# Optimization experiments

Measured on AMD Instinct MI355X. Metric: run time of the kernel, lower is better.

## Reference

```python
import jax, jax.numpy as jnp
import numpy as np

EMB = 1024
HEADS = 16
HEAD_SZ = 64
INNER = 4 * EMB
EPS = 1e-5


def layer_norm(x, g, b):
    mu = jnp.mean(x, axis=-1, keepdims=True)
    var = jnp.mean(jnp.square(x - mu), axis=-1, keepdims=True)
    return (x - mu) * jax.lax.rsqrt(var + EPS) * g + b


def setup_inputs() -> dict:
    key = jax.random.key(0)
    ks = jax.random.split(key, 12)
    s = 1.0 / np.sqrt(EMB)
    si = 1.0 / np.sqrt(INNER)
    return {
        "x": jax.random.normal(ks[0], (4, 2048, EMB), dtype=jnp.float32),
        "Wq": jax.random.uniform(ks[1], (EMB, HEADS * HEAD_SZ), jnp.float32, -s, s),
        "Wk": jax.random.uniform(ks[2], (EMB, HEADS * HEAD_SZ), jnp.float32, -s, s),
        "Wv": jax.random.uniform(ks[3], (EMB, HEADS * HEAD_SZ), jnp.float32, -s, s),
        "Wo": jax.random.uniform(ks[4], (HEADS * HEAD_SZ, EMB), jnp.float32, -s, s),
        "bo": jax.random.uniform(ks[5], (EMB,), jnp.float32, -s, s),
        "g1": jnp.ones((EMB,), jnp.float32),
        "b1": jnp.zeros((EMB,), jnp.float32),
        "W1": jax.random.uniform(ks[6], (EMB, INNER), jnp.float32, -s, s),
        "bf1": jax.random.uniform(ks[7], (INNER,), jnp.float32, -s, s),
        "W2": jax.random.uniform(ks[8], (INNER, EMB), jnp.float32, -si, si),
        "bf2": jax.random.uniform(ks[9], (EMB,), jnp.float32, -si, si),
        "g2": jnp.ones((EMB,), jnp.float32),
        "b2": jnp.zeros((EMB,), jnp.float32),
    }


def reference(x, Wq, Wk, Wv, Wo, bo, g1, b1, W1, bf1, W2, bf2, g2, b2):
    bs, seq, _ = x.shape
    # QKV projections -> [b, h, s, d]
    def split_heads(t):
        return t.reshape(bs, seq, HEADS, HEAD_SZ).transpose(0, 2, 1, 3)
    q = split_heads(x @ Wq)
    k = split_heads(x @ Wk)
    v = split_heads(x @ Wv)
    # scaled dot-product attention (vanilla, no mask; pdrop=0)
    attn = jnp.einsum("bhqd,bhkd->bhqk", q, k) / np.sqrt(HEAD_SZ)
    attn = jax.nn.softmax(attn, axis=-1)
    out = jnp.einsum("bhqk,bhkd->bhqd", attn, v)
    out = out.transpose(0, 2, 1, 3).reshape(bs, seq, HEADS * HEAD_SZ)
    out = out @ Wo + bo
    # residual + post-LN
    h = layer_norm(x + out, g1, b1)
    # FFN
    ff = jax.nn.relu(h @ W1 + bf1) @ W2 + bf2
    return layer_norm(h + ff, g2, b2)
```

## Files before the change

kernel.cpp:

```cpp
#include <hip/hip_runtime.h>
#include <stdint.h>

#define DEVI __device__ __forceinline__

typedef __attribute__((ext_vector_type(8))) short bf16x8;
typedef __attribute__((ext_vector_type(4))) float f32x4;
typedef unsigned short u16;
typedef uint32_t u32;

constexpr int EMB = 1024, SEQ = 2048, NTOK = 8192;
constexpr int HEADS = 16, HD = 64, INNER = 4096;

DEVI u16 f2b(float f) {
  u32 u = __float_as_uint(f);
  return (u16)((u + 0x7FFFu + ((u >> 16) & 1u)) >> 16);
}

DEVI u32 pk2(float lo, float hi) {
  u32 r;
  asm("v_cvt_pk_bf16_f32 %0, %1, %2" : "=v"(r) : "v"(lo), "v"(hi));
  return r;
}

DEVI float exp2v(float x) {
  float r;
  asm("v_exp_f32 %0, %1" : "=v"(r) : "v"(x));
  return r;
}

DEVI void gload16(const void* g, void* l) {
  __builtin_amdgcn_global_load_lds(
      (const __attribute__((address_space(1))) void*)g,
      (__attribute__((address_space(3))) void*)l, 16, 0, 0);
}

DEVI int xcd_swz(int bid, int nwg) { return (bid & 7) * (nwg >> 3) + (bid >> 3); }

DEVI int vperm(int k) {
  int g = (k >> 2) & 3, j = k & 3, s2 = k >> 4;
  return ((s2 >> 1) << 5) + (g << 3) + ((s2 & 1) << 2) + j;
}

__global__ __launch_bounds__(256) void k_cvt(const float* __restrict__ src,
                                             u16* __restrict__ dst, int n4) {
  int i = blockIdx.x * 256 + threadIdx.x;
  if (i >= n4) return;
  float4 v = ((const float4*)src)[i];
  ushort4 o = {f2b(v.x), f2b(v.y), f2b(v.z), f2b(v.w)};
  ((ushort4*)dst)[i] = o;
}

__global__ __launch_bounds__(256) void k_cvtT(const float* __restrict__ src,
                                              u16* __restrict__ dst, int K, int N) {
  __shared__ float t[32][33];
  int bk = blockIdx.x % (K >> 5), bn = blockIdx.x / (K >> 5);
  int tx = threadIdx.x & 31, ty = threadIdx.x >> 5;
#pragma unroll
  for (int i = 0; i < 4; i++)
    t[ty + i * 8][tx] = src[(size_t)(bk * 32 + ty + i * 8) * N + bn * 32 + tx];
  __syncthreads();
#pragma unroll
  for (int i = 0; i < 4; i++)
    dst[(size_t)(bn * 32 + ty + i * 8) * K + bk * 32 + tx] = f2b(t[tx][ty + i * 8]);
}

template <int EPI>
__global__ __launch_bounds__(512, 2) void k_g256(
    const u16* __restrict__ A, const u16* __restrict__ BT, int M, int N, int K,
    u16* __restrict__ ob0, u16* __restrict__ ob1, u16* __restrict__ ob2,
    float* __restrict__ of0, const float* __restrict__ bias,
    const float* __restrict__ res) {
  __shared__ u16 LDS[81920];
  const int tid = threadIdx.x;
  const int lane = tid & 63, w = tid >> 6;
  const int wr = w >> 2, wc = w & 3;
  const int g = lane >> 4, c = lane & 15;
  const int nbx = N >> 8;
  const int bid = xcd_swz(blockIdx.x, gridDim.x);
  const int by = bid / nbx, bx = bid % nbx;
  const int row0 = by << 8, col0 = bx << 8;
  const int NK = K >> 6;

  const f32x4 z4 = {0.f, 0.f, 0.f, 0.f};
  f32x4 acc[8][4];
#pragma unroll
  for (int m = 0; m < 8; m++)
#pragma unroll
    for (int n = 0; n < 4; n++) acc[m][n] = z4;

  auto stA = [&](int t, int h) {
    const int k0 = t << 6;
    char* base = (char*)LDS + (t % 3) * 32768 + h * 16384;
#pragma unroll
    for (int i = 0; i < 2; i++) {
      int s = tid + (i << 9);
      int r = (h << 7) + (s >> 3), cb = s & 7;
      gload16(A + (size_t)(row0 + r) * K + (k0 + ((cb ^ (r & 7)) << 3)),
              base + s * 16);
    }
  };
  auto stB = [&](int t, int h) {
    const int k0 = t << 6;
    char* base = (char*)LDS + 98304 + (t & 1) * 32768 + h * 16384;
#pragma unroll
    for (int i = 0; i < 2; i++) {
      int s = tid + (i << 9);
      int r = (h << 7) + (s >> 3), cb = s & 7;
      gload16(BT + (size_t)(col0 + r) * K + (k0 + ((cb ^ (r & 7)) << 3)),
              base + s * 16);
    }
  };
  auto rdA = [&](const char* Ab, int row, int kk) {
    return *(const bf16x8*)(Ab + ((row * 128 + kk * 64 + g * 16) ^ ((row & 7) << 4)));
  };

  stA(0, 0); stA(0, 1);
  stB(0, 0); stB(0, 1);
  stA(1, 0); stA(1, 1);
  asm volatile("s_waitcnt vmcnt(4)" ::: "memory");
  __builtin_amdgcn_s_barrier();
  __builtin_amdgcn_sched_barrier(0);

  for (int t = 0; t < NK; t++) {
    const char* Ab = (const char*)LDS + (t % 3) * 32768;
    const char* Bb = (const char*)LDS + 98304 + (t & 1) * 32768;
    bf16x8 af[4][2], b0[2][2], b1[2][2];

#pragma unroll
    for (int m = 0; m < 4; m++)
#pragma unroll
      for (int kk = 0; kk < 2; kk++) af[m][kk] = rdA(Ab, wr * 128 + m * 16 + c, kk);
#pragma unroll
    for (int n = 0; n < 2; n++)
#pragma unroll
      for (int kk = 0; kk < 2; kk++) b0[n][kk] = rdA(Bb, wc * 64 + n * 16 + c, kk);
    if (t + 1 < NK) stB(t + 1, 0);
    asm volatile("s_waitcnt lgkmcnt(8)" ::: "memory");
    __builtin_amdgcn_sched_barrier(0);
    __builtin_amdgcn_s_barrier();
    asm volatile("s_waitcnt lgkmcnt(0)" ::: "memory");
    __builtin_amdgcn_sched_barrier(0);
    __builtin_amdgcn_s_setprio(1);
#pragma unroll
    for (int m = 0; m < 4; m++)
#pragma unroll
      for (int n = 0; n < 2; n++)
#pragma unroll
        for (int kk = 0; kk < 2; kk++)
          acc[m][n] = __builtin_amdgcn_mfma_f32_16x16x32_bf16(af[m][kk], b0[n][kk],
                                                              acc[m][n], 0, 0, 0);
    __builtin_amdgcn_s_setprio(0);
    __builtin_amdgcn_sched_barrier(0);
    __builtin_amdgcn_s_barrier();

#pragma unroll
    for (int n = 0; n < 2; n++)
#pragma unroll
      for (int kk = 0; kk < 2; kk++)
        b1[n][kk] = rdA(Bb, wc * 64 + 32 + n * 16 + c, kk);
    if (t + 1 < NK) stB(t + 1, 1);
    __builtin_amdgcn_sched_barrier(0);
    __builtin_amdgcn_s_barrier();
    asm volatile("s_waitcnt lgkmcnt(0)" ::: "memory");
    __builtin_amdgcn_sched_barrier(0);
    __builtin_amdgcn_s_setprio(1);
#pragma unroll
    for (int m = 0; m < 4; m++)
#pragma unroll
      for (int n = 0; n < 2; n++)
#pragma unroll
        for (int kk = 0; kk < 2; kk++)
          acc[m][2 + n] = __builtin_amdgcn_mfma_f32_16x16x32_bf16(af[m][kk], b1[n][kk],
                                                                  acc[m][2 + n], 0, 0, 0);
    __builtin_amdgcn_s_setprio(0);
    __builtin_amdgcn_sched_barrier(0);
    __builtin_amdgcn_s_barrier();

#pragma unroll
    for (int m = 0; m < 4; m++)
#pragma unroll
      for (int kk = 0; kk < 2; kk++)
        af[m][kk] = rdA(Ab, wr * 128 + 64 + m * 16 + c, kk);
    if (t + 2 < NK) stA(t + 2, 0);
    __builtin_amdgcn_sched_barrier(0);
    __builtin_amdgcn_s_barrier();
    asm volatile("s_waitcnt lgkmcnt(0)" ::: "memory");
    __builtin_amdgcn_sched_barrier(0);
    __builtin_amdgcn_s_setprio(1);
#pragma unroll
    for (int m = 0; m < 4; m++)
#pragma unroll
      for (int n = 0; n < 2; n++)
#pragma unroll
        for (int kk = 0; kk < 2; kk++)
          acc[4 + m][n] = __builtin_amdgcn_mfma_f32_16x16x32_bf16(af[m][kk], b0[n][kk],
                                                                  acc[4 + m][n], 0, 0, 0);
    __builtin_amdgcn_s_setprio(0);
    __builtin_amdgcn_sched_barrier(0);
    __builtin_amdgcn_s_barrier();

    if (t + 2 < NK) stA(t + 2, 1);
    __builtin_amdgcn_sched_barrier(0);
    __builtin_amdgcn_s_barrier();
    __builtin_amdgcn_s_setprio(1);
#pragma unroll
    for (int m = 0; m < 4; m++)
#pragma unroll
      for (int n = 0; n < 2; n++)
#pragma unroll
        for (int kk = 0; kk < 2; kk++)
          acc[4 + m][2 + n] = __builtin_amdgcn_mfma_f32_16x16x32_bf16(
              af[m][kk], b1[n][kk], acc[4 + m][2 + n], 0, 0, 0);
    __builtin_amdgcn_s_setprio(0);
    __builtin_amdgcn_sched_barrier(0);
    if (t + 2 < NK)
      asm volatile("s_waitcnt vmcnt(4)" ::: "memory");
    else if (t + 1 < NK)
      asm volatile("s_waitcnt vmcnt(0)" ::: "memory");
    __builtin_amdgcn_s_barrier();
    __builtin_amdgcn_sched_barrier(0);
  }

#pragma unroll
  for (int m = 0; m < 8; m++) {
#pragma unroll
    for (int n = 0; n < 4; n++) {
      int ocol = col0 + wc * 64 + n * 16 + c;
      int orow_base = row0 + wr * 128 + m * 16 + 4 * g;
      if constexpr (EPI == 0) {
        int which = ocol >> 10, rem = ocol & 1023;
        int h = rem >> 6, d = rem & 63;
        if (which == 2) {
          int b = orow_base >> 11, sl = orow_base & 2047;
          int blk = sl & ~63, k4 = sl & 63;
          int p = vperm(k4);
          int bh = b * HEADS + h;
          ushort4 vv = {f2b(acc[m][n][0]), f2b(acc[m][n][1]),
                        f2b(acc[m][n][2]), f2b(acc[m][n][3])};
          *(ushort4*)(ob2 + ((size_t)bh * HD + d) * SEQ + blk + p) = vv;
        } else {
#pragma unroll
          for (int r = 0; r < 4; r++) {
            int orow = orow_base + r;
            int b = orow >> 11, s = orow & 2047;
            int bh = b * HEADS + h;
            float av = acc[m][n][r];
            if (which == 0)
              ob0[((size_t)bh * SEQ + s) * HD + d] = f2b(av * 0.1803368801111244f);
            else
              ob1[((size_t)bh * SEQ + s) * HD + d] = f2b(av);
          }
        }
      } else if constexpr (EPI == 2) {
        float bia = bias[ocol];
#pragma unroll
        for (int r = 0; r < 4; r++) {
          int orow = orow_base + r;
          float v = acc[m][n][r] + bia;
          ob0[(size_t)orow * N + ocol] = f2b(v > 0.f ? v : 0.f);
        }
      } else {
        float bia = bias[ocol];
#pragma unroll
        for (int r = 0; r < 4; r++) {
          int orow = orow_base + r;
          float v = acc[m][n][r] + bia;
          if constexpr (EPI == 1)
            of0[(size_t)orow * N + ocol] = v + res[(size_t)orow * N + ocol];
          else
            of0[(size_t)orow * N + ocol] = v;
        }
      }
    }
  }
}

template <int EPI>
__global__ __launch_bounds__(512, 2) void k_gemm8(
    const u16* __restrict__ A, const u16* __restrict__ BT, int M, int N, int K,
    u16* __restrict__ ob0, u16* __restrict__ ob1, u16* __restrict__ ob2,
    float* __restrict__ of0, const float* __restrict__ bias,
    const float* __restrict__ res) {
  __shared__ u16 LDS[3][24576];
  const int tid = threadIdx.x;
  const int lane = tid & 63, w = tid >> 6;
  const int wr = w >> 1, wc = w & 1;
  const int g = lane >> 4, c = lane & 15;
  const int nbx = N >> 7;
  const int bid = xcd_swz(blockIdx.x, gridDim.x);
  const int by = bid / nbx, bx = bid % nbx;
  const int row0 = by << 8, col0 = bx << 7;
  const int NK = K >> 6;

  const f32x4 z4 = {0.f, 0.f, 0.f, 0.f};
  f32x4 acc[4][4];
#pragma unroll
  for (int m = 0; m < 4; m++)
#pragma unroll
    for (int n = 0; n < 4; n++) acc[m][n] = z4;

  auto stageA = [&](int t) {
    const int k0 = t << 6;
    char* base = (char*)&LDS[t % 3][0];
#pragma unroll
    for (int i = 0; i < 4; i++) {
      int s = tid + (i << 9);
      int r = s >> 3, cb = s & 7;
      gload16(A + (size_t)(row0 + r) * K + (k0 + ((cb ^ (r & 7)) << 3)),
              base + s * 16);
    }
  };
  auto stageB = [&](int t) {
    const int k0 = t << 6;
    char* base = (char*)&LDS[t % 3][0] + 32768;
#pragma unroll
    for (int i = 0; i < 2; i++) {
      int s = tid + (i << 9);
      int r = s >> 3, cb = s & 7;
      gload16(BT + (size_t)(col0 + r) * K + (k0 + ((cb ^ (r & 7)) << 3)),
              base + s * 16);
    }
  };

  stageA(0); stageB(0);
  stageA(1); stageB(1);
  asm volatile("s_waitcnt vmcnt(6)" ::: "memory");
  __builtin_amdgcn_s_barrier();

  for (int t = 0; t < NK; t++) {
    const char* Ab = (const char*)&LDS[t % 3][0];
    const char* Bb = Ab + 32768;

    bf16x8 af[4][2], bfr[2][2];
#pragma unroll
    for (int m = 0; m < 4; m++)
#pragma unroll
      for (int kk = 0; kk < 2; kk++) {
        int r = wr * 64 + m * 16 + c;
        af[m][kk] = *(const bf16x8*)(Ab + ((r * 128 + kk * 64 + g * 16) ^ ((r & 7) << 4)));
      }
#pragma unroll
    for (int ni = 0; ni < 2; ni++)
#pragma unroll
      for (int kk = 0; kk < 2; kk++) {
        int rb = wc * 64 + ni * 16 + c;
        bfr[ni][kk] = *(const bf16x8*)(Bb + ((rb * 128 + kk * 64 + g * 16) ^ ((rb & 7) << 4)));
      }
    if (t + 2 < NK) stageA(t + 2);
    __builtin_amdgcn_sched_barrier(0);
    __builtin_amdgcn_s_barrier();
    asm volatile("s_waitcnt lgkmcnt(0)" ::: "memory");
    __builtin_amdgcn_sched_barrier(0);
    __builtin_amdgcn_s_setprio(1);
#pragma unroll
    for (int m = 0; m < 4; m++)
#pragma unroll
      for (int ni = 0; ni < 2; ni++)
#pragma unroll
        for (int kk = 0; kk < 2; kk++)
          acc[m][ni] = __builtin_amdgcn_mfma_f32_16x16x32_bf16(af[m][kk], bfr[ni][kk],
                                                               acc[m][ni], 0, 0, 0);
    __builtin_amdgcn_s_setprio(0);
    __builtin_amdgcn_sched_barrier(0);
    __builtin_amdgcn_s_barrier();

#pragma unroll
    for (int ni = 0; ni < 2; ni++)
#pragma unroll
      for (int kk = 0; kk < 2; kk++) {
        int rb = wc * 64 + 32 + ni * 16 + c;
        bfr[ni][kk] = *(const bf16x8*)(Bb + ((rb * 128 + kk * 64 + g * 16) ^ ((rb & 7) << 4)));
      }
    if (t + 2 < NK) stageB(t + 2);
    __builtin_amdgcn_sched_barrier(0);
    __builtin_amdgcn_s_barrier();
    asm volatile("s_waitcnt lgkmcnt(0)" ::: "memory");
    __builtin_amdgcn_sched_barrier(0);
    __builtin_amdgcn_s_setprio(1);
#pragma unroll
    for (int m = 0; m < 4; m++)
#pragma unroll
      for (int ni = 0; ni < 2; ni++)
#pragma unroll
        for (int kk = 0; kk < 2; kk++)
          acc[m][2 + ni] = __builtin_amdgcn_mfma_f32_16x16x32_bf16(af[m][kk], bfr[ni][kk],
                                                                   acc[m][2 + ni], 0, 0, 0);
    __builtin_amdgcn_s_setprio(0);
    __builtin_amdgcn_sched_barrier(0);
    if (t + 2 < NK)
      asm volatile("s_waitcnt vmcnt(6)" ::: "memory");
    else if (t + 1 < NK)
      asm volatile("s_waitcnt vmcnt(0)" ::: "memory");
    __builtin_amdgcn_s_barrier();
  }

#pragma unroll
  for (int m = 0; m < 4; m++) {
#pragma unroll
    for (int n = 0; n < 4; n++) {
      int ocol = col0 + wc * 64 + n * 16 + c;
      int orow_base = row0 + wr * 64 + m * 16 + 4 * g;
      if constexpr (EPI == 1) {
        float bia = bias[ocol];
#pragma unroll
        for (int r = 0; r < 4; r++) {
          int orow = orow_base + r;
          of0[(size_t)orow * N + ocol] =
              acc[m][n][r] + bia + res[(size_t)orow * N + ocol];
        }
      } else {
        float bia = bias[ocol];
#pragma unroll
        for (int r = 0; r < 4; r++) {
          int orow = orow_base + r;
          of0[(size_t)orow * N + ocol] = acc[m][n][r] + bia;
        }
      }
    }
  }
}

__global__ __launch_bounds__(256, 4) void k_attn(const u16* __restrict__ q,
                                                 const u16* __restrict__ kb,
                                                 const u16* __restrict__ vT,
                                                 u16* __restrict__ attn) {
  __shared__ u16 Ks[2][64 * 64];
  __shared__ u16 Vs[2][64 * 64];
  const int tid = threadIdx.x, lane = tid & 63, w = tid >> 6;
  const int g = lane >> 4, c = lane & 15;
  const int blk = xcd_swz(blockIdx.x, gridDim.x);
  const int bh = blk >> 5, qb = blk & 31;
  const int b = bh >> 4, h = bh & 15;
  const u16* qh = q + (size_t)bh * SEQ * HD;
  const u16* kh = kb + (size_t)bh * SEQ * HD;
  const u16* vh = vT + (size_t)bh * HD * SEQ;
  const int qr = qb * 64 + w * 16 + c;
  bf16x8 qf0 = *(const bf16x8*)(qh + (size_t)qr * HD + 8 * g);
  bf16x8 qf1 = *(const bf16x8*)(qh + (size_t)qr * HD + 32 + 8 * g);

  const f32x4 z4 = {0.f, 0.f, 0.f, 0.f};
  f32x4 O[4];
#pragma unroll
  for (int m = 0; m < 4; m++) O[m] = z4;
  float mI = -3.0e38f, lI = 0.f;

  auto stage = [&](int kt, int buf) {
    const int kv0 = kt * 64;
#pragma unroll
    for (int i = 0; i < 2; i++) {
      int s = tid + (i << 8);
      int r = s >> 3, cb = s & 7;
      gload16(kh + (size_t)(kv0 + r) * HD + ((cb ^ (r & 7)) << 3),
              (char*)Ks[buf] + s * 16);
    }
#pragma unroll
    for (int i = 0; i < 2; i++) {
      int s = tid + (i << 8);
      int r = s >> 3, cb = s & 7;
      gload16(vh + (size_t)r * SEQ + kv0 + ((cb ^ (r & 7)) << 3),
              (char*)Vs[buf] + s * 16);
    }
  };

  stage(0, 0);
  __syncthreads();
  int cur = 0;
  constexpr int NT = SEQ / 64;
  for (int kt = 0; kt < NT; kt++) {
    if (kt + 1 < NT) stage(kt + 1, cur ^ 1);

    const char* ksb = (const char*)Ks[cur];
    f32x4 sc[4];
    __builtin_amdgcn_s_setprio(1);
#pragma unroll
    for (int m = 0; m < 4; m++) {
      int r = 16 * m + c;
      int sw = (r & 7) << 4;
      bf16x8 kf0 = *(const bf16x8*)(ksb + ((r * 128 + g * 16) ^ sw));
      bf16x8 kf1 = *(const bf16x8*)(ksb + ((r * 128 + 64 + g * 16) ^ sw));
      f32x4 a = z4;
      a = __builtin_amdgcn_mfma_f32_16x16x32_bf16(kf0, qf0, a, 0, 0, 0);
      a = __builtin_amdgcn_mfma_f32_16x16x32_bf16(kf1, qf1, a, 0, 0, 0);
      sc[m] = a;
    }
    __builtin_amdgcn_s_setprio(0);

    float mx = sc[0][0];
#pragma unroll
    for (int m = 0; m < 4; m++)
#pragma unroll
      for (int r = 0; r < 4; r++) mx = fmaxf(mx, sc[m][r]);
    mx = fmaxf(mx, __shfl_xor(mx, 16));
    mx = fmaxf(mx, __shfl_xor(mx, 32));
    if (!__all(mx - mI <= 8.f)) {
      float mNew = fmaxf(mI, mx);
      float alpha = exp2v(mI - mNew);
      lI *= alpha;
#pragma unroll
      for (int m = 0; m < 4; m++)
#pragma unroll
        for (int r = 0; r < 4; r++) O[m][r] *= alpha;
      mI = mNew;
    }
    float p[4][4];
    float rs = 0.f;
#pragma unroll
    for (int m = 0; m < 4; m++)
#pragma unroll
      for (int r = 0; r < 4; r++) {
        p[m][r] = exp2v(sc[m][r] - mI);
        rs += p[m][r];
      }
    rs += __shfl_xor(rs, 16);
    rs += __shfl_xor(rs, 32);
    lI += rs;

    union V8w { bf16x8 v; u32 w4[4]; };
    V8w pa0, pa1;
    pa0.w4[0] = pk2(p[0][0], p[0][1]); pa0.w4[1] = pk2(p[0][2], p[0][3]);
    pa0.w4[2] = pk2(p[1][0], p[1][1]); pa0.w4[3] = pk2(p[1][2], p[1][3]);
    pa1.w4[0] = pk2(p[2][0], p[2][1]); pa1.w4[1] = pk2(p[2][2], p[2][3]);
    pa1.w4[2] = pk2(p[3][0], p[3][1]); pa1.w4[3] = pk2(p[3][2], p[3][3]);

    const char* vsb = (const char*)Vs[cur];
    __builtin_amdgcn_s_setprio(1);
#pragma unroll
    for (int m = 0; m < 4; m++) {
      int d = 16 * m + c;
      int sw = (d & 7) << 4;
      bf16x8 v0 = *(const bf16x8*)(vsb + ((d * 128 + g * 16) ^ sw));
      bf16x8 v1 = *(const bf16x8*)(vsb + ((d * 128 + 64 + g * 16) ^ sw));
      O[m] = __builtin_amdgcn_mfma_f32_16x16x32_bf16(v0, pa0.v, O[m], 0, 0, 0);
      O[m] = __builtin_amdgcn_mfma_f32_16x16x32_bf16(v1, pa1.v, O[m], 0, 0, 0);
    }
    __builtin_amdgcn_s_setprio(0);

    __syncthreads();
    cur ^= 1;
  }

  float inv = 1.f / lI;
#pragma unroll
  for (int m = 0; m < 4; m++) {
    ushort4 ov = {f2b(O[m][0] * inv), f2b(O[m][1] * inv),
                  f2b(O[m][2] * inv), f2b(O[m][3] * inv)};
    int col = h * 64 + 16 * m + 4 * g;
    *(ushort4*)(attn + ((size_t)(b * SEQ + qr)) * EMB + col) = ov;
  }
}

__global__ __launch_bounds__(256) void k_ln1(const float* __restrict__ y,
                                             const float* __restrict__ gw,
                                             const float* __restrict__ bw,
                                             float* __restrict__ hf,
                                             u16* __restrict__ hb) {
  const int row = blockIdx.x, tid = threadIdx.x, lane = tid & 63, w = tid >> 6;
  const float4 v = ((const float4*)(y + (size_t)row * EMB))[tid];
  float s = v.x + v.y + v.z + v.w;
  float s2 = v.x * v.x + v.y * v.y + v.z * v.z + v.w * v.w;
#pragma unroll
  for (int m = 1; m < 64; m <<= 1) {
    s += __shfl_xor(s, m);
    s2 += __shfl_xor(s2, m);
  }
  __shared__ float rs_[4], rq_[4];
  if (lane == 0) { rs_[w] = s; rq_[w] = s2; }
  __syncthreads();
  s = rs_[0] + rs_[1] + rs_[2] + rs_[3];
  s2 = rq_[0] + rq_[1] + rq_[2] + rq_[3];
  const float mu = s * (1.f / EMB);
  const float var = s2 * (1.f / EMB) - mu * mu;
  const float rstd = rsqrtf(var + 1e-5f);
  const float4 gg = ((const float4*)gw)[tid];
  const float4 bb = ((const float4*)bw)[tid];
  float4 o;
  o.x = (v.x - mu) * rstd * gg.x + bb.x;
  o.y = (v.y - mu) * rstd * gg.y + bb.y;
  o.z = (v.z - mu) * rstd * gg.z + bb.z;
  o.w = (v.w - mu) * rstd * gg.w + bb.w;
  ((float4*)(hf + (size_t)row * EMB))[tid] = o;
  ushort4 ob = {f2b(o.x), f2b(o.y), f2b(o.z), f2b(o.w)};
  ((ushort4*)(hb + (size_t)row * EMB))[tid] = ob;
}

__global__ __launch_bounds__(256) void k_ln2(const float* __restrict__ hf,
                                             const float* __restrict__ z,
                                             const float* __restrict__ gw,
                                             const float* __restrict__ bw,
                                             float* __restrict__ outp) {
  const int row = blockIdx.x, tid = threadIdx.x, lane = tid & 63, w = tid >> 6;
  float4 v = ((const float4*)(hf + (size_t)row * EMB))[tid];
  const float4 zz = ((const float4*)(z + (size_t)row * EMB))[tid];
  v.x += zz.x; v.y += zz.y; v.z += zz.z; v.w += zz.w;
  float s = v.x + v.y + v.z + v.w;
  float s2 = v.x * v.x + v.y * v.y + v.z * v.z + v.w * v.w;
#pragma unroll
  for (int m = 1; m < 64; m <<= 1) {
    s += __shfl_xor(s, m);
    s2 += __shfl_xor(s2, m);
  }
  __shared__ float rs_[4], rq_[4];
  if (lane == 0) { rs_[w] = s; rq_[w] = s2; }
  __syncthreads();
  s = rs_[0] + rs_[1] + rs_[2] + rs_[3];
  s2 = rq_[0] + rq_[1] + rq_[2] + rq_[3];
  const float mu = s * (1.f / EMB);
  const float var = s2 * (1.f / EMB) - mu * mu;
  const float rstd = rsqrtf(var + 1e-5f);
  const float4 gg = ((const float4*)gw)[tid];
  const float4 bb = ((const float4*)bw)[tid];
  float4 o;
  o.x = (v.x - mu) * rstd * gg.x + bb.x;
  o.y = (v.y - mu) * rstd * gg.y + bb.y;
  o.z = (v.z - mu) * rstd * gg.z + bb.z;
  o.w = (v.w - mu) * rstd * gg.w + bb.w;
  ((float4*)(outp + (size_t)row * EMB))[tid] = o;
}

extern "C" void kernel_launch(void* const* d_in, const int* in_sizes, int n_in,
                              void* d_out, int out_size, void* d_ws, size_t ws_size,
                              hipStream_t stream) {
  const float* x = (const float*)d_in[0];
  const float* Wq = (const float*)d_in[1];
  const float* Wk = (const float*)d_in[2];
  const float* Wv = (const float*)d_in[3];
  const float* Wo = (const float*)d_in[4];
  const float* bo = (const float*)d_in[5];
  const float* g1 = (const float*)d_in[6];
  const float* b1 = (const float*)d_in[7];
  const float* W1 = (const float*)d_in[8];
  const float* bf1 = (const float*)d_in[9];
  const float* W2 = (const float*)d_in[10];
  const float* bf2 = (const float*)d_in[11];
  const float* g2 = (const float*)d_in[12];
  const float* b2 = (const float*)d_in[13];
  float* out = (float*)d_out;

  char* ws = (char*)d_ws;
  size_t off = 0;
  auto alloc = [&](size_t bytes) {
    char* p = ws + off;
    off += (bytes + 255) & ~(size_t)255;
    return p;
  };
  u16* xb = (u16*)alloc((size_t)NTOK * EMB * 2);
  u16* wqkvT = (u16*)alloc((size_t)3072 * 1024 * 2);
  u16* qB = (u16*)alloc((size_t)NTOK * EMB * 2);
  u16* kB = (u16*)alloc((size_t)NTOK * EMB * 2);
  u16* vTB = (u16*)alloc((size_t)NTOK * EMB * 2);
  u16* woT = (u16*)alloc((size_t)1024 * 1024 * 2);
  u16* w1T = (u16*)alloc((size_t)4096 * 1024 * 2);
  u16* w2T = (u16*)alloc((size_t)1024 * 4096 * 2);
  float* y = (float*)alloc((size_t)NTOK * EMB * 4);
  u16* ff1 = (u16*)alloc((size_t)NTOK * INNER * 2);
  u16* attn = xb;
  float* hf = (float*)qB;
  u16* hb = vTB;
  float* z = y;

  k_cvt<<<NTOK * EMB / 4 / 256, 256, 0, stream>>>(x, xb, NTOK * EMB / 4);
  k_cvtT<<<1024, 256, 0, stream>>>(Wq, wqkvT, 1024, 1024);
  k_cvtT<<<1024, 256, 0, stream>>>(Wk, wqkvT + 1048576, 1024, 1024);
  k_cvtT<<<1024, 256, 0, stream>>>(Wv, wqkvT + 2097152, 1024, 1024);
  k_cvtT<<<1024, 256, 0, stream>>>(Wo, woT, 1024, 1024);
  k_cvtT<<<4096, 256, 0, stream>>>(W1, w1T, 1024, 4096);
  k_cvtT<<<4096, 256, 0, stream>>>(W2, w2T, 4096, 1024);
  k_g256<0><<<(NTOK / 256) * (3072 / 256), 512, 0, stream>>>(
      xb, wqkvT, NTOK, 3072, 1024, qB, kB, vTB, nullptr, nullptr, nullptr);
  k_attn<<<64 * 32, 256, 0, stream>>>(qB, kB, vTB, attn);
  k_gemm8<1><<<(NTOK / 256) * (1024 / 128), 512, 0, stream>>>(
      attn, woT, NTOK, 1024, 1024, nullptr, nullptr, nullptr, y, bo, x);
  k_ln1<<<NTOK, 256, 0, stream>>>(y, g1, b1, hf, hb);
  k_g256<2><<<(NTOK / 256) * (4096 / 256), 512, 0, stream>>>(
      hb, w1T, NTOK, 4096, 1024, ff1, nullptr, nullptr, nullptr, bf1, nullptr);
  k_gemm8<3><<<(NTOK / 256) * (1024 / 128), 512, 0, stream>>>(
      ff1, w2T, NTOK, 1024, 4096, nullptr, nullptr, nullptr, z, bf2, nullptr);
  k_ln2<<<NTOK, 256, 0, stream>>>(hf, z, g2, b2, out);
}
```

Measured before the change: 534.7 us.

## Merge prep kernels, store residual activations in bf16, and relax GEMM sched barriers

Folds the seven conversion and transpose launches into one k_prep launch. The Wo GEMM now writes x+attn as bf16 instead of fp32, and LN1 no longer writes an fp32 copy of h, so LN2 rebuilds the residual from the bf16 h. This cuts memory traffic at the cost of lower precision in the residual path. It also removes several sched_barriers and an lgkmcnt wait in the 256-tile GEMM, moves the softmax row-sum shuffles out of the attention loop, and rewrites the max reduction as a tree.

```diff
diff --git a/kernel.cpp b/kernel.cpp
--- a/kernel.cpp
+++ b/kernel.cpp
@@ -15,6 +15,7 @@
   u32 u = __float_as_uint(f);
   return (u16)((u + 0x7FFFu + ((u >> 16) & 1u)) >> 16);
 }
+DEVI float b2f(u16 h) { return __uint_as_float(((u32)h) << 16); }
 
 DEVI u32 pk2(float lo, float hi) {
   u32 r;
@@ -41,19 +42,38 @@
   return ((s2 >> 1) << 5) + (g << 3) + ((s2 & 1) << 2) + j;
 }
 
-__global__ __launch_bounds__(256) void k_cvt(const float* __restrict__ src,
-                                             u16* __restrict__ dst, int n4) {
-  int i = blockIdx.x * 256 + threadIdx.x;
-  if (i >= n4) return;
-  float4 v = ((const float4*)src)[i];
-  ushort4 o = {f2b(v.x), f2b(v.y), f2b(v.z), f2b(v.w)};
-  ((ushort4*)dst)[i] = o;
-}
-
-__global__ __launch_bounds__(256) void k_cvtT(const float* __restrict__ src,
-                                              u16* __restrict__ dst, int K, int N) {
+__global__ __launch_bounds__(256) void k_prep(
+    const float* __restrict__ x, const float* __restrict__ Wq,
+    const float* __restrict__ Wk, const float* __restrict__ Wv,
+    const float* __restrict__ Wo, const float* __restrict__ W1,
+    const float* __restrict__ W2, u16* __restrict__ xb, u16* __restrict__ wqkvT,
+    u16* __restrict__ woT, u16* __restrict__ w1T, u16* __restrict__ w2T) {
   __shared__ float t[32][33];
-  int bk = blockIdx.x % (K >> 5), bn = blockIdx.x / (K >> 5);
+  int b = blockIdx.x;
+  if (b < 8192) {
+    int i = b * 256 + threadIdx.x;
+    float4 v = ((const float4*)x)[i];
+    ushort4 o = {f2b(v.x), f2b(v.y), f2b(v.z), f2b(v.w)};
+    ((ushort4*)xb)[i] = o;
+    return;
+  }
+  b -= 8192;
+  const float* src;
+  u16* dst;
+  int K, N;
+  if (b < 4096) {
+    int m = b >> 10;
+    b &= 1023;
+    K = 1024; N = 1024;
+    src = (m == 0) ? Wq : (m == 1) ? Wk : (m == 2) ? Wv : Wo;
+    dst = (m == 0) ? wqkvT : (m == 1) ? wqkvT + 1048576
+        : (m == 2) ? wqkvT + 2097152 : woT;
+  } else if (b < 8192) {
+    b -= 4096; src = W1; dst = w1T; K = 1024; N = 4096;
+  } else {
+    b -= 8192; src = W2; dst = w2T; K = 4096; N = 1024;
+  }
+  int bk = b % (K >> 5), bn = b / (K >> 5);
   int tx = threadIdx.x & 31, ty = threadIdx.x >> 5;
 #pragma unroll
   for (int i = 0; i < 4; i++)
@@ -119,7 +139,6 @@
   stA(1, 0); stA(1, 1);
   asm volatile("s_waitcnt vmcnt(4)" ::: "memory");
   __builtin_amdgcn_s_barrier();
-  __builtin_amdgcn_sched_barrier(0);
 
   for (int t = 0; t < NK; t++) {
     const char* Ab = (const char*)LDS + (t % 3) * 32768;
@@ -135,8 +154,6 @@
 #pragma unroll
       for (int kk = 0; kk < 2; kk++) b0[n][kk] = rdA(Bb, wc * 64 + n * 16 + c, kk);
     if (t + 1 < NK) stB(t + 1, 0);
-    asm volatile("s_waitcnt lgkmcnt(8)" ::: "memory");
-    __builtin_amdgcn_sched_barrier(0);
     __builtin_amdgcn_s_barrier();
     asm volatile("s_waitcnt lgkmcnt(0)" ::: "memory");
     __builtin_amdgcn_sched_barrier(0);
@@ -150,7 +167,6 @@
           acc[m][n] = __builtin_amdgcn_mfma_f32_16x16x32_bf16(af[m][kk], b0[n][kk],
                                                               acc[m][n], 0, 0, 0);
     __builtin_amdgcn_s_setprio(0);
-    __builtin_amdgcn_sched_barrier(0);
     __builtin_amdgcn_s_barrier();
 
 #pragma unroll
@@ -159,7 +175,6 @@
       for (int kk = 0; kk < 2; kk++)
         b1[n][kk] = rdA(Bb, wc * 64 + 32 + n * 16 + c, kk);
     if (t + 1 < NK) stB(t + 1, 1);
-    __builtin_amdgcn_sched_barrier(0);
     __builtin_amdgcn_s_barrier();
     asm volatile("s_waitcnt lgkmcnt(0)" ::: "memory");
     __builtin_amdgcn_sched_barrier(0);
@@ -173,7 +188,6 @@
           acc[m][2 + n] = __builtin_amdgcn_mfma_f32_16x16x32_bf16(af[m][kk], b1[n][kk],
                                                                   acc[m][2 + n], 0, 0, 0);
     __builtin_amdgcn_s_setprio(0);
-    __builtin_amdgcn_sched_barrier(0);
     __builtin_amdgcn_s_barrier();
 
 #pragma unroll
@@ -182,7 +196,6 @@
       for (int kk = 0; kk < 2; kk++)
         af[m][kk] = rdA(Ab, wr * 128 + 64 + m * 16 + c, kk);
     if (t + 2 < NK) stA(t + 2, 0);
-    __builtin_amdgcn_sched_barrier(0);
     __builtin_amdgcn_s_barrier();
     asm volatile("s_waitcnt lgkmcnt(0)" ::: "memory");
     __builtin_amdgcn_sched_barrier(0);
@@ -196,11 +209,9 @@
           acc[4 + m][n] = __builtin_amdgcn_mfma_f32_16x16x32_bf16(af[m][kk], b0[n][kk],
                                                                   acc[4 + m][n], 0, 0, 0);
     __builtin_amdgcn_s_setprio(0);
-    __builtin_amdgcn_sched_barrier(0);
     __builtin_amdgcn_s_barrier();
 
     if (t + 2 < NK) stA(t + 2, 1);
-    __builtin_amdgcn_sched_barrier(0);
     __builtin_amdgcn_s_barrier();
     __builtin_amdgcn_s_setprio(1);
 #pragma unroll
@@ -212,13 +223,11 @@
           acc[4 + m][2 + n] = __builtin_amdgcn_mfma_f32_16x16x32_bf16(
               af[m][kk], b1[n][kk], acc[4 + m][2 + n], 0, 0, 0);
     __builtin_amdgcn_s_setprio(0);
-    __builtin_amdgcn_sched_barrier(0);
     if (t + 2 < NK)
       asm volatile("s_waitcnt vmcnt(4)" ::: "memory");
     else if (t + 1 < NK)
       asm volatile("s_waitcnt vmcnt(0)" ::: "memory");
     __builtin_amdgcn_s_barrier();
-    __builtin_amdgcn_sched_barrier(0);
   }
 
 #pragma unroll
@@ -251,7 +260,7 @@
               ob1[((size_t)bh * SEQ + s) * HD + d] = f2b(av);
           }
         }
-      } else if constexpr (EPI == 2) {
+      } else {
         float bia = bias[ocol];
 #pragma unroll
         for (int r = 0; r < 4; r++) {
@@ -259,17 +268,6 @@
           float v = acc[m][n][r] + bia;
           ob0[(size_t)orow * N + ocol] = f2b(v > 0.f ? v : 0.f);
         }
-      } else {
-        float bia = bias[ocol];
-#pragma unroll
-        for (int r = 0; r < 4; r++) {
-          int orow = orow_base + r;
-          float v = acc[m][n][r] + bia;
-          if constexpr (EPI == 1)
-            of0[(size_t)orow * N + ocol] = v + res[(size_t)orow * N + ocol];
-          else
-            of0[(size_t)orow * N + ocol] = v;
-        }
       }
     }
   }
@@ -278,8 +276,7 @@
 template <int EPI>
 __global__ __launch_bounds__(512, 2) void k_gemm8(
     const u16* __restrict__ A, const u16* __restrict__ BT, int M, int N, int K,
-    u16* __restrict__ ob0, u16* __restrict__ ob1, u16* __restrict__ ob2,
-    float* __restrict__ of0, const float* __restrict__ bias,
+    u16* __restrict__ ob0, float* __restrict__ of0, const float* __restrict__ bias,
     const float* __restrict__ res) {
   __shared__ u16 LDS[3][24576];
   const int tid = threadIdx.x;
@@ -400,21 +397,15 @@
     for (int n = 0; n < 4; n++) {
       int ocol = col0 + wc * 64 + n * 16 + c;
       int orow_base = row0 + wr * 64 + m * 16 + 4 * g;
-      if constexpr (EPI == 1) {
-        float bia = bias[ocol];
-#pragma unroll
-        for (int r = 0; r < 4; r++) {
-          int orow = orow_base + r;
-          of0[(size_t)orow * N + ocol] =
-              acc[m][n][r] + bia + res[(size_t)orow * N + ocol];
-        }
-      } else {
-        float bia = bias[ocol];
-#pragma unroll
-        for (int r = 0; r < 4; r++) {
-          int orow = orow_base + r;
+      float bia = bias[ocol];
+#pragma unroll
+      for (int r = 0; r < 4; r++) {
+        int orow = orow_base + r;
+        if constexpr (EPI == 1)
+          ob0[(size_t)orow * N + ocol] =
+              f2b(acc[m][n][r] + bia + res[(size_t)orow * N + ocol]);
+        else
           of0[(size_t)orow * N + ocol] = acc[m][n][r] + bia;
-        }
       }
     }
   }
@@ -485,11 +476,14 @@
     }
     __builtin_amdgcn_s_setprio(0);
 
-    float mx = sc[0][0];
-#pragma unroll
-    for (int m = 0; m < 4; m++)
-#pragma unroll
-      for (int r = 0; r < 4; r++) mx = fmaxf(mx, sc[m][r]);
+    float a0 = fmaxf(fmaxf(sc[0][0], sc[0][1]), sc[0][2]);
+    float a1 = fmaxf(fmaxf(sc[0][3], sc[1][0]), sc[1][1]);
+    float a2 = fmaxf(fmaxf(sc[1][2], sc[1][3]), sc[2][0]);
+    float a3 = fmaxf(fmaxf(sc[2][1], sc[2][2]), sc[2][3]);
+    float a4 = fmaxf(fmaxf(sc[3][0], sc[3][1]), sc[3][2]);
+    float b0 = fmaxf(fmaxf(a0, a1), a2);
+    float b1 = fmaxf(fmaxf(a3, a4), sc[3][3]);
+    float mx = fmaxf(b0, b1);
     mx = fmaxf(mx, __shfl_xor(mx, 16));
     mx = fmaxf(mx, __shfl_xor(mx, 32));
     if (!__all(mx - mI <= 8.f)) {
@@ -511,8 +505,6 @@
         p[m][r] = exp2v(sc[m][r] - mI);
         rs += p[m][r];
       }
-    rs += __shfl_xor(rs, 16);
-    rs += __shfl_xor(rs, 32);
     lI += rs;
 
     union V8w { bf16x8 v; u32 w4[4]; };
@@ -539,6 +531,8 @@
     cur ^= 1;
   }
 
+  lI += __shfl_xor(lI, 16);
+  lI += __shfl_xor(lI, 32);
   float inv = 1.f / lI;
 #pragma unroll
   for (int m = 0; m < 4; m++) {
@@ -549,15 +543,49 @@
   }
 }
 
-__global__ __launch_bounds__(256) void k_ln1(const float* __restrict__ y,
+__global__ __launch_bounds__(256) void k_ln1(const u16* __restrict__ y,
                                              const float* __restrict__ gw,
                                              const float* __restrict__ bw,
-                                             float* __restrict__ hf,
                                              u16* __restrict__ hb) {
   const int row = blockIdx.x, tid = threadIdx.x, lane = tid & 63, w = tid >> 6;
-  const float4 v = ((const float4*)(y + (size_t)row * EMB))[tid];
-  float s = v.x + v.y + v.z + v.w;
-  float s2 = v.x * v.x + v.y * v.y + v.z * v.z + v.w * v.w;
+  ushort4 u = ((const ushort4*)(y + (size_t)row * EMB))[tid];
+  float vx = b2f(u.x), vy = b2f(u.y), vz = b2f(u.z), vw = b2f(u.w);
+  float s = vx + vy + vz + vw;
+  float s2 = vx * vx + vy * vy + vz * vz + vw * vw;
+#pragma unroll
+  for (int m = 1; m < 64; m <<= 1) {
+    s += __shfl_xor(s, m);
+    s2 += __shfl_xor(s2, m);
+  }
+  __shared__ float rs_[4], rq_[4];
+  if (lane == 0) { rs_[w] = s; rq_[w] = s2; }
+  __syncthreads();
+  s = rs_[0] + rs_[1] + rs_[2] + rs_[3];
+  s2 = rq_[0] + rq_[1] + rq_[2] + rq_[3];
+  const float mu = s * (1.f / EMB);
+  const float var = s2 * (1.f / EMB) - mu * mu;
+  const float rstd = rsqrtf(var + 1e-5f);
+  const float4 gg = ((const float4*)gw)[tid];
+  const float4 bb = ((const float4*)bw)[tid];
+  ushort4 ob = {f2b((vx - mu) * rstd * gg.x + bb.x),
+                f2b((vy - mu) * rstd * gg.y + bb.y),
+                f2b((vz - mu) * rstd * gg.z + bb.z),
+                f2b((vw - mu) * rstd * gg.w + bb.w)};
+  ((ushort4*)(hb + (size_t)row * EMB))[tid] = ob;
+}
+
+__global__ __launch_bounds__(256) void k_ln2(const u16* __restrict__ hb,
+                                             const float* __restrict__ z,
+                                             const float* __restrict__ gw,
+                                             const float* __restrict__ bw,
+                                             float* __restrict__ outp) {
+  const int row = blockIdx.x, tid = threadIdx.x, lane = tid & 63, w = tid >> 6;
+  ushort4 u = ((const ushort4*)(hb + (size_t)row * EMB))[tid];
+  const float4 zz = ((const float4*)(z + (size_t)row * EMB))[tid];
+  float vx = b2f(u.x) + zz.x, vy = b2f(u.y) + zz.y;
+  float vz = b2f(u.z) + zz.z, vw = b2f(u.w) + zz.w;
+  float s = vx + vy + vz + vw;
+  float s2 = vx * vx + vy * vy + vz * vz + vw * vw;
 #pragma unroll
   for (int m = 1; m < 64; m <<= 1) {
     s += __shfl_xor(s, m);
@@ -574,46 +602,10 @@
   const float4 gg = ((const float4*)gw)[tid];
   const float4 bb = ((const float4*)bw)[tid];
   float4 o;
-  o.x = (v.x - mu) * rstd * gg.x + bb.x;
-  o.y = (v.y - mu) * rstd * gg.y + bb.y;
-  o.z = (v.z - mu) * rstd * gg.z + bb.z;
-  o.w = (v.w - mu) * rstd * gg.w + bb.w;
-  ((float4*)(hf + (size_t)row * EMB))[tid] = o;
-  ushort4 ob = {f2b(o.x), f2b(o.y), f2b(o.z), f2b(o.w)};
-  ((ushort4*)(hb + (size_t)row * EMB))[tid] = ob;
-}
-
-__global__ __launch_bounds__(256) void k_ln2(const float* __restrict__ hf,
-                                             const float* __restrict__ z,
-                                             const float* __restrict__ gw,
-                                             const float* __restrict__ bw,
-                                             float* __restrict__ outp) {
-  const int row = blockIdx.x, tid = threadIdx.x, lane = tid & 63, w = tid >> 6;
-  float4 v = ((const float4*)(hf + (size_t)row * EMB))[tid];
-  const float4 zz = ((const float4*)(z + (size_t)row * EMB))[tid];
-  v.x += zz.x; v.y += zz.y; v.z += zz.z; v.w += zz.w;
-  float s = v.x + v.y + v.z + v.w;
-  float s2 = v.x * v.x + v.y * v.y + v.z * v.z + v.w * v.w;
-#pragma unroll
-  for (int m = 1; m < 64; m <<= 1) {
-    s += __shfl_xor(s, m);
-    s2 += __shfl_xor(s2, m);
-  }
-  __shared__ float rs_[4], rq_[4];
-  if (lane == 0) { rs_[w] = s; rq_[w] = s2; }
-  __syncthreads();
-  s = rs_[0] + rs_[1] + rs_[2] + rs_[3];
-  s2 = rq_[0] + rq_[1] + rq_[2] + rq_[3];
-  const float mu = s * (1.f / EMB);
-  const float var = s2 * (1.f / EMB) - mu * mu;
-  const float rstd = rsqrtf(var + 1e-5f);
-  const float4 gg = ((const float4*)gw)[tid];
-  const float4 bb = ((const float4*)bw)[tid];
-  float4 o;
-  o.x = (v.x - mu) * rstd * gg.x + bb.x;
-  o.y = (v.y - mu) * rstd * gg.y + bb.y;
-  o.z = (v.z - mu) * rstd * gg.z + bb.z;
-  o.w = (v.w - mu) * rstd * gg.w + bb.w;
+  o.x = (vx - mu) * rstd * gg.x + bb.x;
+  o.y = (vy - mu) * rstd * gg.y + bb.y;
+  o.z = (vz - mu) * rstd * gg.z + bb.z;
+  o.w = (vw - mu) * rstd * gg.w + bb.w;
   ((float4*)(outp + (size_t)row * EMB))[tid] = o;
 }
 
@@ -651,29 +643,23 @@
   u16* woT = (u16*)alloc((size_t)1024 * 1024 * 2);
   u16* w1T = (u16*)alloc((size_t)4096 * 1024 * 2);
   u16* w2T = (u16*)alloc((size_t)1024 * 4096 * 2);
-  float* y = (float*)alloc((size_t)NTOK * EMB * 4);
+  u16* y = (u16*)alloc((size_t)NTOK * EMB * 2);
   u16* ff1 = (u16*)alloc((size_t)NTOK * INNER * 2);
   u16* attn = xb;
-  float* hf = (float*)qB;
+  float* z = (float*)qB;
   u16* hb = vTB;
-  float* z = y;
-
-  k_cvt<<<NTOK * EMB / 4 / 256, 256, 0, stream>>>(x, xb, NTOK * EMB / 4);
-  k_cvtT<<<1024, 256, 0, stream>>>(Wq, wqkvT, 1024, 1024);
-  k_cvtT<<<1024, 256, 0, stream>>>(Wk, wqkvT + 1048576, 1024, 1024);
-  k_cvtT<<<1024, 256, 0, stream>>>(Wv, wqkvT + 2097152, 1024, 1024);
-  k_cvtT<<<1024, 256, 0, stream>>>(Wo, woT, 1024, 1024);
-  k_cvtT<<<4096, 256, 0, stream>>>(W1, w1T, 1024, 4096);
-  k_cvtT<<<4096, 256, 0, stream>>>(W2, w2T, 4096, 1024);
+
+  k_prep<<<20480, 256, 0, stream>>>(x, Wq, Wk, Wv, Wo, W1, W2, xb, wqkvT, woT,
+                                    w1T, w2T);
   k_g256<0><<<(NTOK / 256) * (3072 / 256), 512, 0, stream>>>(
       xb, wqkvT, NTOK, 3072, 1024, qB, kB, vTB, nullptr, nullptr, nullptr);
   k_attn<<<64 * 32, 256, 0, stream>>>(qB, kB, vTB, attn);
   k_gemm8<1><<<(NTOK / 256) * (1024 / 128), 512, 0, stream>>>(
-      attn, woT, NTOK, 1024, 1024, nullptr, nullptr, nullptr, y, bo, x);
-  k_ln1<<<NTOK, 256, 0, stream>>>(y, g1, b1, hf, hb);
+      attn, woT, NTOK, 1024, 1024, y, nullptr, bo, x);
+  k_ln1<<<NTOK, 256, 0, stream>>>(y, g1, b1, hb);
   k_g256<2><<<(NTOK / 256) * (4096 / 256), 512, 0, stream>>>(
       hb, w1T, NTOK, 4096, 1024, ff1, nullptr, nullptr, nullptr, bf1, nullptr);
   k_gemm8<3><<<(NTOK / 256) * (1024 / 128), 512, 0, stream>>>(
-      ff1, w2T, NTOK, 1024, 4096, nullptr, nullptr, nullptr, z, bf2, nullptr);
-  k_ln2<<<NTOK, 256, 0, stream>>>(hf, z, g2, b2, out);
-}
+      ff1, w2T, NTOK, 1024, 4096, nullptr, z, bf2, nullptr);
+  k_ln2<<<NTOK, 256, 0, stream>>>(hb, z, g2, b2, out);
+}
```

After: 509.8 us. -4.7%, faster.
